# Kernel tuning notes

Hardware: AMD Instinct MI355X
Metric: run time of the kernel (lower is better)

The kernel has to match this reference:

```python
import jax, jax.numpy as jnp
import numpy as np

HEADS, DIM, N = 16, 128, 2048
NEG = -1e9


def setup_inputs() -> dict:
    key = jax.random.key(0)
    ks = jax.random.split(key, 8)
    xavier = lambda k, shape, fan: jax.random.uniform(
        k, shape, jnp.float32, -1.0, 1.0) * np.sqrt(6.0 / fan)
    return {
        "q": jax.random.normal(ks[0], (N, DIM), jnp.float32),
        "k": jax.random.normal(ks[1], (N, DIM), jnp.float32),
        "v": jax.random.normal(ks[2], (N, DIM), jnp.float32),
        "mask": jax.random.randint(ks[3], (N, N), 0, 2) > 0,
        "Q": xavier(ks[4], (HEADS, DIM, DIM), 2 * DIM),
        "K": xavier(ks[5], (HEADS, DIM, DIM), 2 * DIM),
        "V": xavier(ks[6], (HEADS, DIM, DIM), 2 * DIM),
        "last": xavier(ks[7], (HEADS * DIM, DIM), HEADS * DIM + DIM),
    }


def reference(q, k, v, Q, K, V, last, mask):
    # per-head projections: [n, d] x [h, d, d] -> [h, n, d]
    qp = jnp.einsum('nd,hde->hne', q, Q)
    kp = jnp.einsum('nd,hde->hne', k, K)
    vp = jnp.einsum('nd,hde->hne', v, V)
    n = qp.shape[1]
    # NOTE: original computes k @ q^T and scales by sqrt(seq_len) (q.size(1) after projection)
    att = jnp.einsum('hid,hjd->hij', kp, qp)  # [h, n, n]
    fmask = mask.astype(jnp.float32)
    att = att * fmask / jnp.sqrt(jnp.float32(n)) + NEG * (1.0 - fmask)
    att = jax.nn.softmax(att, axis=2)
    out = jnp.einsum('hij,hjd->hid', att, vp)            # [h, n, d]
    out = jnp.transpose(out, (1, 0, 2)).reshape(n, -1)   # n (heads d)
    return out @ last
```

## Files before the change

kernel.cpp:

```cpp
#include <hip/hip_runtime.h>
#include <hip/hip_bf16.h>


#define HN 16
#define NN 2048
#define DD 128

typedef __attribute__((ext_vector_type(8))) short short8;
typedef __attribute__((ext_vector_type(4))) short short4v;
typedef __attribute__((ext_vector_type(4))) float float4v;
typedef __attribute__((ext_vector_type(16))) float f32x16;
typedef __attribute__((ext_vector_type(4))) unsigned int uint4v;

#define CROW(r) ((((r) & 3)) + 8 * ((r) >> 2))

__device__ inline unsigned short f2bf(float f) {
    unsigned int u = __builtin_bit_cast(unsigned int, f);
    unsigned int r = (u + 0x7fffu + ((u >> 16) & 1u)) >> 16;
    return (unsigned short)r;
}

__device__ inline unsigned int cvtpk(float lo, float hi) {
    unsigned int w;
    asm("v_cvt_pk_bf16_f32 %0, %1, %2" : "=v"(w) : "v"(lo), "v"(hi));
    return w;
}

__device__ inline void plswap(unsigned int& x, unsigned int& y) {
#if __has_builtin(__builtin_amdgcn_permlane32_swap)
    typedef int int2v __attribute__((ext_vector_type(2)));
    int2v r = __builtin_amdgcn_permlane32_swap((int)x, (int)y, false, false);
    x = (unsigned int)r[0];
    y = (unsigned int)r[1];
#else
    const unsigned int sx = (unsigned int)__shfl_xor((int)x, 32);
    const unsigned int sy = (unsigned int)__shfl_xor((int)y, 32);
    const bool hiHalf = (threadIdx.x & 32) != 0;
    const unsigned int nx = hiHalf ? sy : x;
    const unsigned int ny = hiHalf ? y : sx;
    x = nx; y = ny;
#endif
}

__device__ inline short8 ld_bf8(const float* __restrict__ p) {
    const float4v a = *(const float4v*)p;
    const float4v b = *(const float4v*)(p + 4);
    short8 r;
    r[0] = (short)f2bf(a[0]); r[1] = (short)f2bf(a[1]);
    r[2] = (short)f2bf(a[2]); r[3] = (short)f2bf(a[3]);
    r[4] = (short)f2bf(b[0]); r[5] = (short)f2bf(b[1]);
    r[6] = (short)f2bf(b[2]); r[7] = (short)f2bf(b[3]);
    return r;
}

__device__ inline short8 ld2x4(const unsigned short* p) {
    const short4v lo = *(const short4v*)p;
    const short4v hi = *(const short4v*)(p + 4);
    short8 r;
    r[0] = lo[0]; r[1] = lo[1]; r[2] = lo[2]; r[3] = lo[3];
    r[4] = hi[0]; r[5] = hi[1]; r[6] = hi[2]; r[7] = hi[3];
    return r;
}

__global__ void sentinel_kernel(float* out, int n) {
    int i = blockIdx.x * 256 + threadIdx.x;
    if (i < n) out[i] = 2.0f;
}

__global__ __launch_bounds__(256) void zero_kernel(float* __restrict__ out, int n) {
    const int i4 = blockIdx.x * 256 + threadIdx.x;
    if (i4 * 4 + 3 < n) {
        *(float4v*)(out + i4 * 4) = float4v{0.f, 0.f, 0.f, 0.f};
    } else {
        for (int i = i4 * 4; i < n; i++) out[i] = 0.f;
    }
}

__global__ __launch_bounds__(256) void maskpack_kernel(
    const int* __restrict__ mask,
    unsigned long long* __restrict__ mb)
{
    const int word = blockIdx.x * 4 + (threadIdx.x >> 6);
    const int lane = threadIdx.x & 63;
    const int i = word >> 5;
    const int w = word & 31;
    const int mv = mask[(size_t)i * NN + w * 64 + lane];
    const unsigned long long b = __ballot(mv != 0);
    if (lane == 0) mb[word] = b;
}

__global__ __launch_bounds__(256) void wprep_kernel(
    const float* __restrict__ Qw,
    const float* __restrict__ Kw,
    const float* __restrict__ Vw,
    unsigned short* __restrict__ wsW)
{
    __shared__ __align__(16) unsigned short Wt[128 * 132];
    const int h = blockIdx.x, t = blockIdx.y;
    const float* W = ((t == 0) ? Qw : ((t == 1) ? Kw : Vw)) + h * DD * DD;
    unsigned short* o = wsW + ((size_t)t * HN + h) * DD * DD;
    const int tid = threadIdx.x;

    for (int idx2 = tid * 2; idx2 < DD * DD; idx2 += 512) {
        const int d = idx2 >> 7, e = idx2 & 127;
        const float2 w2 = *(const float2*)(W + idx2);
        Wt[(e + 0) * 132 + d] = f2bf(w2.x);
        Wt[(e + 1) * 132 + d] = f2bf(w2.y);
    }
    __syncthreads();
    for (int idx8 = tid * 8; idx8 < DD * DD; idx8 += 2048) {
        const int e = idx8 >> 7, d = idx8 & 127;
        *(short8*)(o + idx8) = ld2x4(&Wt[e * 132 + d]);
    }
}

__global__ __launch_bounds__(256) void proj3_kernel(
    const float* __restrict__ q,
    const float* __restrict__ k,
    const float* __restrict__ v,
    const unsigned short* __restrict__ wsW,
    unsigned short* __restrict__ ws)
{
    __shared__ __align__(16) unsigned short Wt[128 * 136];
    const int t = blockIdx.z, h = blockIdx.y, cb = blockIdx.x;
    const int tid = threadIdx.x;
    const float* in = (t == 0) ? q : ((t == 1) ? k : v);
    const unsigned short* WTg = wsW + ((size_t)t * HN + h) * DD * DD;
    unsigned short* out = ws + (size_t)t * (HN * NN * DD) + (size_t)h * (NN * DD);

#pragma unroll
    for (int it = 0; it < 8; it++) {
        const int idx8 = tid * 8 + it * 2048;
        const int row = idx8 >> 7, col = idx8 & 127;
        *(short8*)(&Wt[row * 136 + col]) = *(const short8*)(WTg + idx8);
    }
    __syncthreads();

    const int wave = tid >> 6, lane = tid & 63;
    const int quad = lane >> 4, l16 = lane & 15;

#pragma unroll 1
    for (int rt = 0; rt < 2; rt++) {
        const int row0 = cb * 128 + rt * 64 + wave * 16;

        float4v acc[8];
#pragma unroll
        for (int c = 0; c < 8; c++) acc[c] = {0.f, 0.f, 0.f, 0.f};

        if (t < 2) {
#pragma unroll
            for (int kk = 0; kk < 4; kk++) {
                const short8 a = ld_bf8(in + (size_t)(row0 + l16) * DD + kk * 32 + quad * 8);
#pragma unroll
                for (int c = 0; c < 8; c++) {
                    const short8 b = *(const short8*)(&Wt[(c * 16 + l16) * 136 + kk * 32 + quad * 8]);
                    acc[c] = __builtin_amdgcn_mfma_f32_16x16x32_bf16(a, b, acc[c], 0, 0, 0);
                }
            }
#pragma unroll
            for (int c = 0; c < 8; c++)
#pragma unroll
                for (int r = 0; r < 4; r++)
                    out[(size_t)(row0 + quad * 4 + r) * DD + c * 16 + l16] = f2bf(acc[c][r]);
        } else {
#pragma unroll
            for (int kk = 0; kk < 4; kk++) {
                const short8 bv = ld_bf8(in + (size_t)(row0 + l16) * DD + kk * 32 + quad * 8);
#pragma unroll
                for (int c = 0; c < 8; c++) {
                    const short8 aw = *(const short8*)(&Wt[(c * 16 + l16) * 136 + kk * 32 + quad * 8]);
                    acc[c] = __builtin_amdgcn_mfma_f32_16x16x32_bf16(aw, bv, acc[c], 0, 0, 0);
                }
            }
#pragma unroll
            for (int c = 0; c < 8; c++)
#pragma unroll
                for (int r = 0; r < 4; r++)
                    out[(size_t)(c * 16 + quad * 4 + r) * NN + row0 + l16] = f2bf(acc[c][r]);
        }
    }
}

__global__ __launch_bounds__(256, 2) void attn_kernel(
    unsigned short* __restrict__ ws,
    const unsigned long long* __restrict__ mb)
{
    __shared__ __align__(16) unsigned short qs[2][64 * 136];
    __shared__ __align__(16) unsigned short vpTile[2][128 * 72];

    const int h = blockIdx.y, ib = blockIdx.x;
    const int tid = threadIdx.x;
    const int wave = tid >> 6, lane = tid & 63;
    const int ig = wave >> 1;
    const int h2 = wave & 1;
    const int l31 = lane & 31;
    const int hi = lane >> 5;

    const unsigned short* qp  = ws + (size_t)h * (NN * DD);
    const unsigned short* kp  = ws + (size_t)(HN * NN * DD) + (size_t)h * (NN * DD);
    const unsigned short* vpT = ws + (size_t)(2 * HN * NN * DD) + (size_t)h * (NN * DD);
    unsigned short* ao = ws + (size_t)(3 * HN * NN * DD);

    const int i0 = ib * 64;
    const float scale = 0.022097086912079612f;

    short8 kpf[8];
    {
        const int row = i0 + ig * 32 + l31;
#pragma unroll
        for (int kk = 0; kk < 8; kk++)
            kpf[kk] = *(const short8*)(kp + (size_t)row * DD + kk * 16 + hi * 8);
    }

    short8 rq[4], rv[4];

#define LOADT(J0) do {                                                         \
        _Pragma("unroll")                                                      \
        for (int it = 0; it < 4; it++) {                                       \
            const int idx = tid * 8 + it * 2048;                               \
            rq[it] = *(const short8*)(qp + (size_t)(J0) * DD + idx);           \
            rv[it] = *(const short8*)(vpT + (size_t)(idx >> 6) * NN + (J0) + (idx & 63)); \
        } } while (0)

#define WRITET(BUF) do {                                                       \
        _Pragma("unroll")                                                      \
        for (int it = 0; it < 4; it++) {                                       \
            const int idx = tid * 8 + it * 2048;                               \
            *(short8*)(&qs[BUF][(idx >> 7) * 136 + (idx & 127)]) = rq[it];     \
            *(short8*)(&vpTile[BUF][(idx >> 6) * 72 + (idx & 63)]) = rv[it];   \
        } } while (0)

    f32x16 o[4];
#pragma unroll
    for (int dt = 0; dt < 4; dt++)
#pragma unroll
        for (int r = 0; r < 16; r++) o[dt][r] = 0.f;
    float lacc = 0.f;

    auto COMPUTE = [&](int buf, int jt) {
        const unsigned long long mrow = mb[(size_t)(i0 + ig * 32 + l31) * 32 + jt];
        const unsigned int m2 = (unsigned int)(mrow >> (h2 * 32 + hi * 4));

        f32x16 s;
#pragma unroll
        for (int r = 0; r < 16; r++) s[r] = 0.f;
#pragma unroll
        for (int kk = 0; kk < 8; kk++) {
            const short8 aq = *(const short8*)(&qs[buf][(h2 * 32 + l31) * 136 + kk * 16 + hi * 8]);
            s = __builtin_amdgcn_mfma_f32_32x32x16_bf16(aq, kpf[kk], s, 0, 0, 0);
        }

#pragma unroll
        for (int r = 0; r < 16; r++) {
            const float x = ((m2 >> CROW(r)) & 1u) ? fmaf(s[r], scale, -5.0f) : -50.0f;
            s[r] = __expf(x);
        }
        float ls = (((s[0] + s[1]) + (s[2] + s[3])) + ((s[4] + s[5]) + (s[6] + s[7])))
                 + (((s[8] + s[9]) + (s[10] + s[11])) + ((s[12] + s[13]) + (s[14] + s[15])));
        ls += __shfl_xor(ls, 32);
        lacc += ls;

        short8 pa[2];
#pragma unroll
        for (int ks = 0; ks < 2; ks++) {
            const int b = ks * 8;
            unsigned int x0 = cvtpk(s[b + 0], s[b + 1]);
            unsigned int y0 = cvtpk(s[b + 4], s[b + 5]);
            unsigned int x1 = cvtpk(s[b + 2], s[b + 3]);
            unsigned int y1 = cvtpk(s[b + 6], s[b + 7]);
            plswap(x0, y0);
            plswap(x1, y1);
            uint4v w; w[0] = x0; w[1] = x1; w[2] = y0; w[3] = y1;
            pa[ks] = __builtin_bit_cast(short8, w);
        }

#pragma unroll
        for (int ks = 0; ks < 2; ks++) {
#pragma unroll
            for (int dt = 0; dt < 4; dt++) {
                const short8 bv = *(const short8*)(&vpTile[buf][(dt * 32 + l31) * 72 + h2 * 32 + ks * 16 + hi * 8]);
                o[dt] = __builtin_amdgcn_mfma_f32_32x32x16_bf16(pa[ks], bv, o[dt], 0, 0, 0);
            }
        }
    };

    LOADT(0);
    WRITET(0);
    LOADT(64);
    __syncthreads();

    int cur = 0;

#pragma unroll 1
    for (int jt = 0; jt < 30; ++jt) {
        WRITET(cur ^ 1);
        LOADT((jt + 2) * 64);
        COMPUTE(cur, jt);
        __syncthreads();
        cur ^= 1;
    }
    WRITET(cur ^ 1);
    COMPUTE(cur, 30);
    __syncthreads();
    cur ^= 1;
    COMPUTE(cur, 31);

#undef LOADT
#undef WRITET

    __syncthreads();
    float* obuf = (float*)&qs[0][0];
    float* lbuf = (float*)&vpTile[0][0];

    if (h2 == 1) {
#pragma unroll
        for (int dt = 0; dt < 4; dt++)
#pragma unroll
            for (int r = 0; r < 16; r++)
                obuf[(((ig * 2 + hi) * 4 + dt) * 16 + r) * 32 + l31] = o[dt][r];
        if (hi == 0) lbuf[ig * 32 + l31] = lacc;
    }
    __syncthreads();
    if (h2 == 0) {
        const float lt = lacc + lbuf[ig * 32 + l31];
        const float inv = (lt > 0.f) ? (1.0f / lt) : 0.f;
        if (hi == 0) lbuf[64 + ig * 32 + l31] = inv;
#pragma unroll
        for (int dt = 0; dt < 4; dt++)
#pragma unroll
            for (int r = 0; r < 16; r++) {
                const int row = CROW(r) + hi * 4;
                const float val = (o[dt][r] + obuf[(((ig * 2 + hi) * 4 + dt) * 16 + r) * 32 + l31])
                                  * lbuf[64 + ig * 32 + row];
                ao[(size_t)(i0 + ig * 32 + row) * (HN * DD) + h * DD + dt * 32 + l31] = f2bf(val);
            }
    }
}

__global__ __launch_bounds__(256) void final2_kernel(
    const unsigned short* __restrict__ ao,
    const float* __restrict__ last,
    float* __restrict__ outp)
{
    __shared__ __align__(16) unsigned short lt[32 * 516];
    const int tid = threadIdx.x;
    const int wave = tid >> 6, lane = tid & 63;
    const int quad = lane >> 4, l16 = lane & 15;
    const int i0 = blockIdx.x * 64;
    const int e0 = blockIdx.y * 32;
    const int k0 = blockIdx.z * 512;

#pragma unroll
    for (int idx2 = tid * 2; idx2 < 512 * 32; idx2 += 512) {
        const int kk = idx2 >> 5, e = idx2 & 31;
        const float2 w2 = *(const float2*)(last + (size_t)(k0 + kk) * DD + e0 + e);
        lt[(e + 0) * 516 + kk] = f2bf(w2.x);
        lt[(e + 1) * 516 + kk] = f2bf(w2.y);
    }
    __syncthreads();

    float4v acc[2];
    acc[0] = {0.f, 0.f, 0.f, 0.f};
    acc[1] = {0.f, 0.f, 0.f, 0.f};

    const unsigned short* arow = ao + (size_t)(i0 + wave * 16 + l16) * (HN * DD) + k0;

#pragma unroll
    for (int kb = 0; kb < 8; kb++) {
#pragma unroll
        for (int ks = 0; ks < 2; ks++) {
            const short8 a = *(const short8*)(arow + kb * 64 + ks * 32 + quad * 8);
#pragma unroll
            for (int dc = 0; dc < 2; dc++) {
                const short8 b = ld2x4(&lt[(dc * 16 + l16) * 516 + kb * 64 + ks * 32 + quad * 8]);
                acc[dc] = __builtin_amdgcn_mfma_f32_16x16x32_bf16(a, b, acc[dc], 0, 0, 0);
            }
        }
    }

#pragma unroll
    for (int r = 0; r < 4; r++)
#pragma unroll
        for (int dc = 0; dc < 2; dc++)
            atomicAdd(&outp[(size_t)(i0 + wave * 16 + quad * 4 + r) * DD + e0 + dc * 16 + l16],
                      acc[dc][r]);
}

extern "C" void kernel_launch(void* const* d_in, const int* in_sizes, int n_in,
                              void* d_out, int out_size, void* d_ws, size_t ws_size,
                              hipStream_t stream)
{
    const float* q    = (const float*)d_in[0];
    const float* k    = (const float*)d_in[1];
    const float* v    = (const float*)d_in[2];
    const int*   mask = (const int*)d_in[3];
    const float* Qw   = (const float*)d_in[4];
    const float* Kw   = (const float*)d_in[5];
    const float* Vw   = (const float*)d_in[6];
    const float* last = (const float*)d_in[7];
    unsigned short* ws  = (unsigned short*)d_ws;
    float* out = (float*)d_out;

    const size_t shorts_main = (size_t)4 * HN * NN * DD;
    const size_t mb_bytes = (size_t)NN * (NN / 64) * 8;
    const size_t needed = shorts_main * sizeof(unsigned short) + mb_bytes;
    if (ws_size < needed) {
        sentinel_kernel<<<(out_size + 255) / 256, 256, 0, stream>>>(out, out_size);
        return;
    }
    unsigned long long* mb = (unsigned long long*)(ws + shorts_main);
    unsigned short* wsW = ws + (size_t)3 * HN * NN * DD;

    zero_kernel<<<dim3((out_size / 4 + 255) / 256), 256, 0, stream>>>(out, out_size);
    maskpack_kernel<<<dim3(NN * (NN / 64) / 4), 256, 0, stream>>>(mask, mb);
    wprep_kernel<<<dim3(16, 3), 256, 0, stream>>>(Qw, Kw, Vw, wsW);
    proj3_kernel<<<dim3(16, 16, 3), 256, 0, stream>>>(q, k, v, wsW, ws);
    attn_kernel<<<dim3(32, 16), 256, 0, stream>>>(ws, mb);
    final2_kernel<<<dim3(32, 4, 4), 256, 0, stream>>>(ws + (size_t)3 * HN * NN * DD, last, out);
}
```

Measured before the change: 165.2 us.

## Fuse output zeroing into mask packing, add MFMA priority and lighter LDS barriers

The zero kernel is merged into a mask-packing kernel in which each wave packs four 64-bit mask words, so one launch disappears. The attention loop raises wave priority around its MFMA blocks with s_setprio. It also replaces __syncthreads with a barrier that waits only on LDS counters, so in-flight global prefetch loads do not stall the barrier. The risks are that zeroing now depends on the 4096-block grid covering out_size (2048*128 = 262144 fits), and that the barrier change depends on the global loads not being needed before the next iteration.

```diff
diff --git a/kernel.cpp b/kernel.cpp
--- a/kernel.cpp
+++ b/kernel.cpp
@@ -42,6 +42,13 @@
 #endif
 }
 
+__device__ inline void bar_lds() {
+    asm volatile("s_waitcnt lgkmcnt(0)" ::: "memory");
+    __builtin_amdgcn_sched_barrier(0);
+    __builtin_amdgcn_s_barrier();
+    __builtin_amdgcn_sched_barrier(0);
+}
+
 __device__ inline short8 ld_bf8(const float* __restrict__ p) {
     const float4v a = *(const float4v*)p;
     const float4v b = *(const float4v*)(p + 4);
@@ -67,26 +74,27 @@
     if (i < n) out[i] = 2.0f;
 }
 
-__global__ __launch_bounds__(256) void zero_kernel(float* __restrict__ out, int n) {
-    const int i4 = blockIdx.x * 256 + threadIdx.x;
-    if (i4 * 4 + 3 < n) {
-        *(float4v*)(out + i4 * 4) = float4v{0.f, 0.f, 0.f, 0.f};
-    } else {
-        for (int i = i4 * 4; i < n; i++) out[i] = 0.f;
-    }
-}
-
-__global__ __launch_bounds__(256) void maskpack_kernel(
+__global__ __launch_bounds__(256) void maskpack2_kernel(
     const int* __restrict__ mask,
-    unsigned long long* __restrict__ mb)
-{
-    const int word = blockIdx.x * 4 + (threadIdx.x >> 6);
+    unsigned long long* __restrict__ mb,
+    float* __restrict__ out, int out_n)
+{
+    const int wgrp = blockIdx.x * 4 + (threadIdx.x >> 6);
     const int lane = threadIdx.x & 63;
-    const int i = word >> 5;
-    const int w = word & 31;
-    const int mv = mask[(size_t)i * NN + w * 64 + lane];
-    const unsigned long long b = __ballot(mv != 0);
-    if (lane == 0) mb[word] = b;
+    const int word0 = wgrp * 4;
+    const int i = word0 >> 5;
+    const int w = word0 & 31;
+    const int* row = mask + (size_t)i * NN + w * 64;
+    unsigned long long b[4];
+#pragma unroll
+    for (int c = 0; c < 4; c++)
+        b[c] = __ballot(row[c * 64 + lane] != 0);
+    if (lane == 0) {
+#pragma unroll
+        for (int c = 0; c < 4; c++) mb[word0 + c] = b[c];
+    }
+    const int z = blockIdx.x * 256 + threadIdx.x;
+    if (z < out_n) out[z] = 0.f;
 }
 
 __global__ __launch_bounds__(256) void wprep_kernel(
@@ -244,11 +252,13 @@
         f32x16 s;
 #pragma unroll
         for (int r = 0; r < 16; r++) s[r] = 0.f;
+        __builtin_amdgcn_s_setprio(1);
 #pragma unroll
         for (int kk = 0; kk < 8; kk++) {
             const short8 aq = *(const short8*)(&qs[buf][(h2 * 32 + l31) * 136 + kk * 16 + hi * 8]);
             s = __builtin_amdgcn_mfma_f32_32x32x16_bf16(aq, kpf[kk], s, 0, 0, 0);
         }
+        __builtin_amdgcn_s_setprio(0);
 
 #pragma unroll
         for (int r = 0; r < 16; r++) {
@@ -274,6 +284,7 @@
             pa[ks] = __builtin_bit_cast(short8, w);
         }
 
+        __builtin_amdgcn_s_setprio(1);
 #pragma unroll
         for (int ks = 0; ks < 2; ks++) {
 #pragma unroll
@@ -282,6 +293,7 @@
                 o[dt] = __builtin_amdgcn_mfma_f32_32x32x16_bf16(pa[ks], bv, o[dt], 0, 0, 0);
             }
         }
+        __builtin_amdgcn_s_setprio(0);
     };
 
     LOADT(0);
@@ -296,12 +308,12 @@
         WRITET(cur ^ 1);
         LOADT((jt + 2) * 64);
         COMPUTE(cur, jt);
-        __syncthreads();
+        bar_lds();
         cur ^= 1;
     }
     WRITET(cur ^ 1);
     COMPUTE(cur, 30);
-    __syncthreads();
+    bar_lds();
     cur ^= 1;
     COMPUTE(cur, 31);
 
@@ -411,8 +423,7 @@
     unsigned long long* mb = (unsigned long long*)(ws + shorts_main);
     unsigned short* wsW = ws + (size_t)3 * HN * NN * DD;
 
-    zero_kernel<<<dim3((out_size / 4 + 255) / 256), 256, 0, stream>>>(out, out_size);
-    maskpack_kernel<<<dim3(NN * (NN / 64) / 4), 256, 0, stream>>>(mask, mb);
+    maskpack2_kernel<<<dim3(NN * (NN / 64) / 16), 256, 0, stream>>>(mask, mb, out, out_size);
     wprep_kernel<<<dim3(16, 3), 256, 0, stream>>>(Qw, Kw, Vw, wsW);
     proj3_kernel<<<dim3(16, 16, 3), 256, 0, stream>>>(q, k, v, wsW, ws);
     attn_kernel<<<dim3(32, 16), 256, 0, stream>>>(ws, mb);
```

Result: faster. 161.6 us (-2.2%).
